# Performance work log

Hardware: AMD Instinct MI355X
Metric: run time of the kernel (lower is better)

## Reference

```python
import jax, jax.numpy as jnp
import numpy as np

N_NODES = 50000
N_EDGES = 800000
NFEAT, NHID, NCLASS = 512, 128, 40
BN_EPS = 1e-5


def setup_inputs() -> dict:
    key = jax.random.key(0)
    ks = jax.random.split(key, 12)
    x = jax.random.normal(ks[0], (N_NODES, NFEAT), dtype=jnp.float32)
    edge_index = jax.random.randint(ks[1], (2, N_EDGES), 0, N_NODES, dtype=jnp.int64)
    edge_weight = jax.random.uniform(ks[2], (N_EDGES,), dtype=jnp.float32)
    def glorot(k, fi, fo):
        lim = (6.0 / (fi + fo)) ** 0.5
        return jax.random.uniform(k, (fi, fo), minval=-lim, maxval=lim, dtype=jnp.float32)
    return {
        "x": x, "edge_index": edge_index, "edge_weight": edge_weight,
        "W1": glorot(ks[3], NFEAT, NHID), "b1": jnp.zeros((NHID,), jnp.float32),
        "W2": glorot(ks[4], NHID, NHID), "b2": jnp.zeros((NHID,), jnp.float32),
        "W3": glorot(ks[5], NHID, NHID), "b3": jnp.zeros((NHID,), jnp.float32),
        "g1": jnp.ones((NHID,), jnp.float32), "be1": jnp.zeros((NHID,), jnp.float32),
        "g2": jnp.ones((NHID,), jnp.float32), "be2": jnp.zeros((NHID,), jnp.float32),
        "g3": jnp.ones((NHID,), jnp.float32), "be3": jnp.zeros((NHID,), jnp.float32),
        "linW": glorot(ks[6], NHID, NCLASS), "linb": jnp.zeros((NCLASS,), jnp.float32),
    }


def _gcn_norm(edge_index, edge_weight, n):
    # PyG gcn_norm: add self-loops (weight 1), symmetric D^-1/2 (A+I) D^-1/2
    loop = jnp.arange(n, dtype=edge_index.dtype)
    row = jnp.concatenate([edge_index[0], loop])
    col = jnp.concatenate([edge_index[1], loop])
    ew = jnp.concatenate([edge_weight, jnp.ones((n,), edge_weight.dtype)])
    deg = jax.ops.segment_sum(ew, col, num_segments=n)
    dinv = jnp.where(deg > 0, jax.lax.rsqrt(jnp.maximum(deg, 1e-30)), 0.0)
    norm = dinv[row] * ew * dinv[col]
    return row, col, norm


def _conv(x, W, b, row, col, norm, n):
    h = x @ W                                   # [N, out]
    msg = h[row] * norm[:, None]                # gather + weight, [E+N, out]
    return jax.ops.segment_sum(msg, col, num_segments=n) + b


def _bn(x, g, b):
    # training-mode BatchNorm over node dim (biased variance)
    mu = jnp.mean(x, axis=0)
    var = jnp.mean((x - mu) ** 2, axis=0)
    return (x - mu) * jax.lax.rsqrt(var + BN_EPS) * g + b


def reference(x, edge_index, edge_weight, W1, b1, W2, b2, W3, b3,
              g1, be1, g2, be2, g3, be3, linW, linb):
    n = x.shape[0]
    row, col, norm = _gcn_norm(edge_index, edge_weight, n)
    x1 = _bn(jax.nn.relu(_conv(x, W1, b1, row, col, norm, n)), g1, be1)
    x2 = _bn(jax.nn.relu(_conv(x1, W2, b2, row, col, norm, n)), g2, be2)
    x3 = _bn(_conv(x2, W3, b3, row, col, norm, n), g3, be3)
    logits = x3 @ linW + linb
    return (logits, jax.nn.softmax(logits, axis=1), x3)
```

## Files before the change

kernel.cpp:

```cpp
#include <hip/hip_runtime.h>
#include <hip/hip_bf16.h>

#define N_NODES 50000
#define N_EDGES 800000
#define NFEAT 512
#define NHID 128
#define NCLASS 40
#define BN_EPS 1e-5f

typedef __attribute__((ext_vector_type(8))) short short8;
typedef __attribute__((ext_vector_type(4))) float f32x4;

__device__ __forceinline__ unsigned short f2b(float f) {
    unsigned int u = __float_as_uint(f);
    u += 0x7fff + ((u >> 16) & 1);
    return (unsigned short)(u >> 16);
}
__device__ __forceinline__ float blo(unsigned int v) {
    return __uint_as_float(v << 16);
}
__device__ __forceinline__ float bhi(unsigned int v) {
    return __uint_as_float(v & 0xffff0000u);
}

__global__ void k_detect(const unsigned int* __restrict__ words, int* __restrict__ flag) {
    __shared__ int s_any;
    if (threadIdx.x == 0) s_any = 0;
    __syncthreads();
    unsigned int v = words[2 * threadIdx.x + 1];
    if (v != 0) atomicAdd(&s_any, 1);
    __syncthreads();
    if (threadIdx.x == 0) *flag = (s_any == 0) ? 1 : 0;
}

__global__ void k_init_node(unsigned long long* __restrict__ degcnt) {
    int i = blockIdx.x * blockDim.x + threadIdx.x;
    if (i < N_NODES) degcnt[i] = 0ULL;
}

__global__ void k_convert_accum(const unsigned int* __restrict__ words,
                                const int* __restrict__ flag,
                                const float* __restrict__ ew,
                                int* __restrict__ row, int* __restrict__ col,
                                unsigned long long* __restrict__ degcnt,
                                int* __restrict__ slot) {
    int e = blockIdx.x * blockDim.x + threadIdx.x;
    if (e >= N_EDGES) return;
    int f = *flag;
    unsigned int r = f ? words[2 * (size_t)e] : words[e];
    unsigned int c = f ? words[2 * ((size_t)e + N_EDGES)] : words[e + N_EDGES];
    row[e] = (int)r;
    col[e] = (int)c;
    unsigned int q = __float2uint_rn(ew[e] * 8388608.0f);
    unsigned long long old = atomicAdd(&degcnt[c], (1ULL << 32) | (unsigned long long)q);
    slot[e] = (int)(old >> 32);
}

#define SCAN_BLOCKS ((N_NODES + 255) / 256)

__global__ __launch_bounds__(256) void k_dinv(const unsigned long long* __restrict__ degcnt,
                                              float* __restrict__ dinv,
                                              int* __restrict__ counts,
                                              int* __restrict__ bsum) {
    int i = blockIdx.x * 256 + threadIdx.x;
    int cnt = 0;
    if (i < N_NODES) {
        unsigned long long v = degcnt[i];
        float deg = 1.0f + (float)(unsigned int)(v & 0xffffffffULL) * (1.0f / 8388608.0f);
        dinv[i] = rsqrtf(deg);
        cnt = (int)(v >> 32);
        counts[i] = cnt;
    }
    __shared__ int sh[256];
    sh[threadIdx.x] = cnt;
    __syncthreads();
    for (int ofs = 128; ofs > 0; ofs >>= 1) {
        if (threadIdx.x < ofs) sh[threadIdx.x] += sh[threadIdx.x + ofs];
        __syncthreads();
    }
    if (threadIdx.x == 0) bsum[blockIdx.x] = sh[0];
}

__global__ __launch_bounds__(256) void k_scan2(const int* __restrict__ bsum,
                                               int* __restrict__ bpre,
                                               int* __restrict__ colptr) {
    int t = threadIdx.x;
    int v = (t < SCAN_BLOCKS) ? bsum[t] : 0;
    __shared__ int sh[256];
    sh[t] = v;
    __syncthreads();
    for (int ofs = 1; ofs < 256; ofs <<= 1) {
        int u = (t >= ofs) ? sh[t - ofs] : 0;
        __syncthreads();
        sh[t] += u;
        __syncthreads();
    }
    if (t < SCAN_BLOCKS) bpre[t] = sh[t] - v;
    if (t == SCAN_BLOCKS - 1) colptr[N_NODES] = sh[t];
}

__global__ __launch_bounds__(256) void k_scan3(const int* __restrict__ counts,
                                               const int* __restrict__ bpre,
                                               int* __restrict__ colptr) {
    int t = threadIdx.x;
    int i = blockIdx.x * 256 + t;
    int v = (i < N_NODES) ? counts[i] : 0;
    __shared__ int sh[256];
    sh[t] = v;
    __syncthreads();
    for (int ofs = 1; ofs < 256; ofs <<= 1) {
        int u = (t >= ofs) ? sh[t - ofs] : 0;
        __syncthreads();
        sh[t] += u;
        __syncthreads();
    }
    if (i < N_NODES) colptr[i] = bpre[blockIdx.x] + sh[t] - v;
}

__global__ void k_scatter(const int* __restrict__ row, const int* __restrict__ col,
                          const float* __restrict__ ew, const float* __restrict__ dinv,
                          const int* __restrict__ colptr, const int* __restrict__ slot,
                          int2* __restrict__ ern) {
    int e = blockIdx.x * blockDim.x + threadIdx.x;
    if (e < N_EDGES) {
        int c = col[e], r = row[e];
        int p = colptr[c] + slot[e];
        float nrm = dinv[r] * ew[e] * dinv[c];
        ern[p] = make_int2(r, __float_as_int(nrm));
    }
}

__global__ void k_prep_w(const float* __restrict__ W1, const float* __restrict__ W2,
                         const float* __restrict__ W3, unsigned short* __restrict__ W1t,
                         unsigned short* __restrict__ W2t, unsigned short* __restrict__ W3t) {
    int i = blockIdx.x * blockDim.x + threadIdx.x;
    if (i < 65536) {
        int k = i >> 7, n = i & 127;
        W1t[n * 512 + k] = f2b(W1[i]);
    } else if (i < 81920) {
        int j = i - 65536; int k = j >> 7, n = j & 127;
        W2t[n * 128 + k] = f2b(W2[j]);
    } else if (i < 98304) {
        int j = i - 81920; int k = j >> 7, n = j & 127;
        W3t[n * 128 + k] = f2b(W3[j]);
    }
}

template <int K, bool FUSE, bool ABF16>
__global__ __launch_bounds__(256) void k_gemm_bf16(
    const void* __restrict__ Av, const unsigned short* __restrict__ Wt,
    const float* __restrict__ scale, const float* __restrict__ shift,
    unsigned short* __restrict__ Out, int M) {
    __shared__ unsigned short As[128][40];
    __shared__ unsigned short Bs[128][40];
    __shared__ float s_sc[128], s_sh[128];
    int tid = threadIdx.x;
    int m0 = blockIdx.x * 128;
    if (FUSE) {
        if (tid < 128) { s_sc[tid] = scale[tid]; s_sh[tid] = shift[tid]; }
        __syncthreads();
    }
    int srow = tid >> 1;
    int skh = (tid & 1) << 4;
    int wave = tid >> 6, lane = tid & 63;
    int wm = (wave >> 1) * 64, wn = (wave & 1) * 64;
    int l15 = lane & 15, quad = lane >> 4;
    f32x4 acc[4][4] = {};
    bool arow_ok = (m0 + srow) < M;
    const float* arow_f = (const float*)Av + (size_t)(m0 + srow) * K + skh;
    const unsigned int* arow_b = (const unsigned int*)Av + (size_t)(m0 + srow) * (K / 2) + (skh >> 1);
    const unsigned short* wrow_p = Wt + (size_t)srow * K + skh;
    for (int kt = 0; kt < K; kt += 32) {
        unsigned int p[8];
        if (ABF16) {
            uint4 r0 = make_uint4(0, 0, 0, 0), r1 = make_uint4(0, 0, 0, 0);
            if (arow_ok) {
                r0 = *(const uint4*)(arow_b + (kt >> 1));
                r1 = *(const uint4*)(arow_b + (kt >> 1) + 4);
            }
            unsigned int raw[8] = {r0.x, r0.y, r0.z, r0.w, r1.x, r1.y, r1.z, r1.w};
#pragma unroll
            for (int q = 0; q < 8; q++) {
                if (FUSE) {
                    int ch = kt + skh + 2 * q;
                    float f0 = blo(raw[q]) * s_sc[ch] + s_sh[ch];
                    float f1 = bhi(raw[q]) * s_sc[ch + 1] + s_sh[ch + 1];
                    p[q] = (unsigned int)f2b(f0) | ((unsigned int)f2b(f1) << 16);
                } else {
                    p[q] = raw[q];
                }
            }
        } else {
            float v[16];
#pragma unroll
            for (int q = 0; q < 4; q++) {
                float4 t4 = make_float4(0.f, 0.f, 0.f, 0.f);
                if (arow_ok) t4 = *(const float4*)(arow_f + kt + q * 4);
                v[q * 4 + 0] = t4.x; v[q * 4 + 1] = t4.y;
                v[q * 4 + 2] = t4.z; v[q * 4 + 3] = t4.w;
            }
            if (FUSE) {
#pragma unroll
                for (int q = 0; q < 16; q++)
                    v[q] = v[q] * s_sc[kt + skh + q] + s_sh[kt + skh + q];
            }
#pragma unroll
            for (int q = 0; q < 8; q++)
                p[q] = (unsigned int)f2b(v[2 * q]) | ((unsigned int)f2b(v[2 * q + 1]) << 16);
        }
        uint4 w0 = make_uint4(p[0], p[1], p[2], p[3]);
        uint4 w1 = make_uint4(p[4], p[5], p[6], p[7]);
        uint4 b0 = *(const uint4*)(wrow_p + kt);
        uint4 b1 = *(const uint4*)(wrow_p + kt + 8);
        *(uint4*)&As[srow][skh] = w0;
        *(uint4*)&As[srow][skh + 8] = w1;
        *(uint4*)&Bs[srow][skh] = b0;
        *(uint4*)&Bs[srow][skh + 8] = b1;
        __syncthreads();
        short8 a[4], b[4];
#pragma unroll
        for (int i = 0; i < 4; i++) a[i] = *(const short8*)&As[wm + i * 16 + l15][quad * 8];
#pragma unroll
        for (int j = 0; j < 4; j++) b[j] = *(const short8*)&Bs[wn + j * 16 + l15][quad * 8];
#pragma unroll
        for (int i = 0; i < 4; i++)
#pragma unroll
            for (int j = 0; j < 4; j++)
                acc[i][j] = __builtin_amdgcn_mfma_f32_16x16x32_bf16(a[i], b[j], acc[i][j], 0, 0, 0);
        __syncthreads();
    }
#pragma unroll
    for (int i = 0; i < 4; i++) {
        int mb = m0 + wm + i * 16 + quad * 4;
#pragma unroll
        for (int r = 0; r < 4; r++) {
            int m = mb + r;
            if (m < M) {
#pragma unroll
                for (int j = 0; j < 4; j++)
                    Out[(size_t)m * 128 + wn + j * 16 + l15] = f2b(acc[i][j][r]);
            }
        }
    }
}

__global__ __launch_bounds__(256) void k_aggregate(
    const unsigned int* __restrict__ hb, const int* __restrict__ colptr,
    const int2* __restrict__ ern, const float* __restrict__ dinv,
    const float* __restrict__ bias, unsigned int* __restrict__ out, int relu) {
    int node = (blockIdx.x * blockDim.x + threadIdx.x) >> 6;
    int lane = threadIdx.x & 63;
    if (node >= N_NODES) return;
    float di = dinv[node];
    float selfw = di * di;
    unsigned int sv = hb[(size_t)node * 64 + lane];
    float a0 = selfw * blo(sv);
    float a1 = selfw * bhi(sv);
    float c0 = 0.f, c1 = 0.f;
    int e = colptr[node], end = colptr[node + 1];
    for (; e + 8 <= end; e += 8) {
        int2 rw[8];
#pragma unroll
        for (int q = 0; q < 8; q++) rw[q] = ern[e + q];
        unsigned int v[8];
#pragma unroll
        for (int q = 0; q < 8; q++) v[q] = hb[(size_t)rw[q].x * 64 + lane];
#pragma unroll
        for (int q = 0; q < 8; q++) {
            float w = __int_as_float(rw[q].y);
            if (q & 1) { c0 += w * blo(v[q]); c1 += w * bhi(v[q]); }
            else       { a0 += w * blo(v[q]); a1 += w * bhi(v[q]); }
        }
    }
    for (; e < end; e++) {
        int2 rw = ern[e];
        float w = __int_as_float(rw.y);
        unsigned int v = hb[(size_t)rw.x * 64 + lane];
        a0 += w * blo(v);
        a1 += w * bhi(v);
    }
    a0 += c0; a1 += c1;
    float2 bv = *(const float2*)&bias[2 * lane];
    a0 += bv.x;
    a1 += bv.y;
    if (relu) { a0 = fmaxf(a0, 0.f); a1 = fmaxf(a1, 0.f); }
    out[(size_t)node * 64 + lane] = (unsigned int)f2b(a0) | ((unsigned int)f2b(a1) << 16);
}

#define BN_BLOCKS ((N_NODES + 255) / 256)

__global__ __launch_bounds__(256) void k_bnstats(const unsigned int* __restrict__ x,
                                                 float* __restrict__ psum,
                                                 float* __restrict__ psumsq) {
    int u = threadIdx.x & 63;
    int strip = threadIdx.x >> 6;
    int r0 = blockIdx.x * 256;
    int rend = min(r0 + 256, N_NODES);
    float sl = 0.f, s2l = 0.f, sh_ = 0.f, s2h = 0.f;
    for (int r = r0 + strip; r < rend; r += 4) {
        unsigned int v = x[(size_t)r * 64 + u];
        float a = blo(v), b = bhi(v);
        sl += a; s2l += a * a;
        sh_ += b; s2h += b * b;
    }
    __shared__ float buf[4][64][4];
    buf[strip][u][0] = sl; buf[strip][u][1] = s2l;
    buf[strip][u][2] = sh_; buf[strip][u][3] = s2h;
    __syncthreads();
    if (strip == 0) {
#pragma unroll
        for (int s = 1; s < 4; s++) {
            sl += buf[s][u][0]; s2l += buf[s][u][1];
            sh_ += buf[s][u][2]; s2h += buf[s][u][3];
        }
        psum[blockIdx.x * 128 + 2 * u] = sl;
        psum[blockIdx.x * 128 + 2 * u + 1] = sh_;
        psumsq[blockIdx.x * 128 + 2 * u] = s2l;
        psumsq[blockIdx.x * 128 + 2 * u + 1] = s2h;
    }
}

__global__ void k_bnfinal(const float* __restrict__ psum, const float* __restrict__ psumsq,
                          const float* __restrict__ g, const float* __restrict__ be,
                          float* __restrict__ scale, float* __restrict__ shift) {
    int c = threadIdx.x;
    if (c < 128) {
        float s = 0.f, s2 = 0.f;
        for (int b = 0; b < BN_BLOCKS; b++) {
            s += psum[b * 128 + c];
            s2 += psumsq[b * 128 + c];
        }
        const float invn = 1.0f / (float)N_NODES;
        float mu = s * invn;
        float var = s2 * invn - mu * mu;
        float iv = rsqrtf(var + BN_EPS);
        float sc = g[c] * iv;
        scale[c] = sc;
        shift[c] = be[c] - mu * sc;
    }
}

__global__ __launch_bounds__(256) void k_logits(const unsigned int* __restrict__ abuf,
                                                const float* __restrict__ scale,
                                                const float* __restrict__ shift,
                                                const float* __restrict__ linW,
                                                const float* __restrict__ linb,
                                                float* __restrict__ logits,
                                                float* __restrict__ probs,
                                                float* __restrict__ x3out) {
    __shared__ float Xs[64][130];
    __shared__ float Ws[128 * 40];
    __shared__ float s_sc[128], s_sh[128];
    int tid = threadIdx.x;
    int m0 = blockIdx.x * 64;
    if (tid < 128) { s_sc[tid] = scale[tid]; s_sh[tid] = shift[tid]; }
    for (int q = tid; q < 1280; q += 256)
        *(float4*)&Ws[q * 4] = *(const float4*)&linW[q * 4];
    __syncthreads();
    for (int q = tid; q < 4096; q += 256) {
        int r = q >> 6, u = q & 63;
        int m = m0 + r;
        float f0 = 0.f, f1 = 0.f;
        if (m < N_NODES) {
            unsigned int v = abuf[(size_t)m * 64 + u];
            f0 = blo(v) * s_sc[2 * u] + s_sh[2 * u];
            f1 = bhi(v) * s_sc[2 * u + 1] + s_sh[2 * u + 1];
            *(float2*)&x3out[(size_t)m * 128 + 2 * u] = make_float2(f0, f1);
        }
        *(float2*)&Xs[r][2 * u] = make_float2(f0, f1);
    }
    __syncthreads();
    int r = tid >> 2;
    int cg = tid & 3;
    int cbase = cg * 10;
    float acc[10] = {};
    for (int k = 0; k < 128; k++) {
        float a = Xs[r][k];
#pragma unroll
        for (int j = 0; j < 10; j++) acc[j] += a * Ws[k * 40 + cbase + j];
    }
#pragma unroll
    for (int j = 0; j < 10; j++) acc[j] += linb[cbase + j];
    float m = acc[0];
#pragma unroll
    for (int j = 1; j < 10; j++) m = fmaxf(m, acc[j]);
    m = fmaxf(m, __shfl_xor(m, 1));
    m = fmaxf(m, __shfl_xor(m, 2));
    float ex[10];
    float s = 0.f;
#pragma unroll
    for (int j = 0; j < 10; j++) { ex[j] = expf(acc[j] - m); s += ex[j]; }
    s += __shfl_xor(s, 1);
    s += __shfl_xor(s, 2);
    float inv = 1.0f / s;
    int mrow = m0 + r;
    if (mrow < N_NODES) {
#pragma unroll
        for (int j = 0; j < 10; j++) {
            logits[(size_t)mrow * 40 + cbase + j] = acc[j];
            probs[(size_t)mrow * 40 + cbase + j] = ex[j] * inv;
        }
    }
}

extern "C" void kernel_launch(void* const* d_in, const int* in_sizes, int n_in,
                              void* d_out, int out_size, void* d_ws, size_t ws_size,
                              hipStream_t stream) {
    const float* x = (const float*)d_in[0];
    const unsigned int* eidx = (const unsigned int*)d_in[1];
    const float* ew = (const float*)d_in[2];
    const float* W1 = (const float*)d_in[3];
    const float* b1 = (const float*)d_in[4];
    const float* W2 = (const float*)d_in[5];
    const float* b2 = (const float*)d_in[6];
    const float* W3 = (const float*)d_in[7];
    const float* b3 = (const float*)d_in[8];
    const float* g1 = (const float*)d_in[9];
    const float* be1 = (const float*)d_in[10];
    const float* g2 = (const float*)d_in[11];
    const float* be2 = (const float*)d_in[12];
    const float* g3 = (const float*)d_in[13];
    const float* be3 = (const float*)d_in[14];
    const float* linW = (const float*)d_in[15];
    const float* linb = (const float*)d_in[16];

    float* out = (float*)d_out;
    float* logits = out;
    float* probs = out + (size_t)N_NODES * NCLASS;
    float* x3out = out + 2 * (size_t)N_NODES * NCLASS;

    char* ws = (char*)d_ws;
    size_t off = 0;
    auto take = [&](size_t bytes) -> char* {
        char* p = ws + off;
        off += (bytes + 255) & ~(size_t)255;
        return p;
    };
    int* row32 = (int*)take((size_t)N_EDGES * 4);
    int* col32 = (int*)take((size_t)N_EDGES * 4);
    int* slot = (int*)take((size_t)N_EDGES * 4);
    int* colptr = (int*)take((size_t)(N_NODES + 1) * 4);
    int* counts = (int*)take((size_t)N_NODES * 4);
    unsigned long long* degcnt = (unsigned long long*)take((size_t)N_NODES * 8);
    int2* ern = (int2*)take((size_t)N_EDGES * 8);
    float* dinv = (float*)take((size_t)N_NODES * 4);
    unsigned short* hbuf = (unsigned short*)take((size_t)N_NODES * NHID * 2);
    unsigned short* abuf = (unsigned short*)take((size_t)N_NODES * NHID * 2);
    unsigned short* W1t = (unsigned short*)take((size_t)512 * 128 * 2);
    unsigned short* W2t = (unsigned short*)take((size_t)128 * 128 * 2);
    unsigned short* W3t = (unsigned short*)take((size_t)128 * 128 * 2);
    float* psum = (float*)take((size_t)BN_BLOCKS * 128 * 4);
    float* psumsq = (float*)take((size_t)BN_BLOCKS * 128 * 4);
    float* scale = (float*)take(128 * 4);
    float* shift = (float*)take(128 * 4);
    int* bsum = (int*)take((size_t)SCAN_BLOCKS * 4);
    int* bpre = (int*)take((size_t)SCAN_BLOCKS * 4);
    int* flag = (int*)take(4);
    (void)ws_size; (void)n_in; (void)in_sizes; (void)out_size;

    const int TPB = 256;
    int grid_e = (N_EDGES + TPB - 1) / TPB;
    int grid_gemm = (N_NODES + 127) / 128;
    int grid_agg = (N_NODES * 64 + TPB - 1) / TPB;
    int grid_head = (N_NODES + 63) / 64;

    k_detect<<<1, 256, 0, stream>>>(eidx, flag);
    k_init_node<<<SCAN_BLOCKS, TPB, 0, stream>>>(degcnt);
    k_convert_accum<<<grid_e, TPB, 0, stream>>>(eidx, flag, ew, row32, col32, degcnt, slot);
    k_dinv<<<SCAN_BLOCKS, TPB, 0, stream>>>(degcnt, dinv, counts, bsum);
    k_scan2<<<1, TPB, 0, stream>>>(bsum, bpre, colptr);
    k_scan3<<<SCAN_BLOCKS, TPB, 0, stream>>>(counts, bpre, colptr);
    k_scatter<<<grid_e, TPB, 0, stream>>>(row32, col32, ew, dinv, colptr, slot, ern);
    k_prep_w<<<(98304 + TPB - 1) / TPB, TPB, 0, stream>>>(W1, W2, W3, W1t, W2t, W3t);

    k_gemm_bf16<NFEAT, false, false><<<grid_gemm, TPB, 0, stream>>>(x, W1t, nullptr, nullptr, hbuf, N_NODES);
    k_aggregate<<<grid_agg, TPB, 0, stream>>>((const unsigned int*)hbuf, colptr, ern, dinv, b1, (unsigned int*)abuf, 1);
    k_bnstats<<<BN_BLOCKS, TPB, 0, stream>>>((const unsigned int*)abuf, psum, psumsq);
    k_bnfinal<<<1, 128, 0, stream>>>(psum, psumsq, g1, be1, scale, shift);

    k_gemm_bf16<NHID, true, true><<<grid_gemm, TPB, 0, stream>>>(abuf, W2t, scale, shift, hbuf, N_NODES);
    k_aggregate<<<grid_agg, TPB, 0, stream>>>((const unsigned int*)hbuf, colptr, ern, dinv, b2, (unsigned int*)abuf, 1);
    k_bnstats<<<BN_BLOCKS, TPB, 0, stream>>>((const unsigned int*)abuf, psum, psumsq);
    k_bnfinal<<<1, 128, 0, stream>>>(psum, psumsq, g2, be2, scale, shift);

    k_gemm_bf16<NHID, true, true><<<grid_gemm, TPB, 0, stream>>>(abuf, W3t, scale, shift, hbuf, N_NODES);
    k_aggregate<<<grid_agg, TPB, 0, stream>>>((const unsigned int*)hbuf, colptr, ern, dinv, b3, (unsigned int*)abuf, 0);
    k_bnstats<<<BN_BLOCKS, TPB, 0, stream>>>((const unsigned int*)abuf, psum, psumsq);
    k_bnfinal<<<1, 128, 0, stream>>>(psum, psumsq, g3, be3, scale, shift);

    k_logits<<<grid_head, TPB, 0, stream>>>((const unsigned int*)abuf, scale, shift, linW, linb, logits, probs, x3out);
}
```

Before: 526.0 us.

## Fuse GEMM1 with edge conversion, atomic BN stats, fold BN finalize into consumers

Merges the first-layer GEMM and the edge-index conversion/degree accumulation into one launch with block-range dispatch, so the independent graph-preprocessing work can overlap the dense GEMM. The separate detect kernel is folded into each edge block, which repeats the format probe per block. BN statistics now go through float atomics into a single 128-wide sum buffer zeroed by the aggregate kernel, and the per-channel scale/shift finalize is recomputed inside the next GEMM and the logits kernel. This removes the bnfinal launches and partial-sum buffers, at the cost of atomic contention and order-dependent float summation.

Result: faster. 494.6 us (-6.0%).

```diff
diff --git a/kernel.cpp b/kernel.cpp
--- a/kernel.cpp
+++ b/kernel.cpp
@@ -11,6 +11,11 @@
 typedef __attribute__((ext_vector_type(8))) short short8;
 typedef __attribute__((ext_vector_type(4))) float f32x4;
 
+#define GEMM1_BLOCKS ((N_NODES + 127) / 128)
+#define EDGE_BLOCKS ((N_EDGES + 255) / 256)
+#define SCAN_BLOCKS ((N_NODES + 255) / 256)
+#define BN_BLOCKS ((N_NODES + 255) / 256)
+
 __device__ __forceinline__ unsigned short f2b(float f) {
     unsigned int u = __float_as_uint(f);
     u += 0x7fff + ((u >> 16) & 1);
@@ -23,111 +28,9 @@
     return __uint_as_float(v & 0xffff0000u);
 }
 
-__global__ void k_detect(const unsigned int* __restrict__ words, int* __restrict__ flag) {
-    __shared__ int s_any;
-    if (threadIdx.x == 0) s_any = 0;
-    __syncthreads();
-    unsigned int v = words[2 * threadIdx.x + 1];
-    if (v != 0) atomicAdd(&s_any, 1);
-    __syncthreads();
-    if (threadIdx.x == 0) *flag = (s_any == 0) ? 1 : 0;
-}
-
 __global__ void k_init_node(unsigned long long* __restrict__ degcnt) {
     int i = blockIdx.x * blockDim.x + threadIdx.x;
     if (i < N_NODES) degcnt[i] = 0ULL;
-}
-
-__global__ void k_convert_accum(const unsigned int* __restrict__ words,
-                                const int* __restrict__ flag,
-                                const float* __restrict__ ew,
-                                int* __restrict__ row, int* __restrict__ col,
-                                unsigned long long* __restrict__ degcnt,
-                                int* __restrict__ slot) {
-    int e = blockIdx.x * blockDim.x + threadIdx.x;
-    if (e >= N_EDGES) return;
-    int f = *flag;
-    unsigned int r = f ? words[2 * (size_t)e] : words[e];
-    unsigned int c = f ? words[2 * ((size_t)e + N_EDGES)] : words[e + N_EDGES];
-    row[e] = (int)r;
-    col[e] = (int)c;
-    unsigned int q = __float2uint_rn(ew[e] * 8388608.0f);
-    unsigned long long old = atomicAdd(&degcnt[c], (1ULL << 32) | (unsigned long long)q);
-    slot[e] = (int)(old >> 32);
-}
-
-#define SCAN_BLOCKS ((N_NODES + 255) / 256)
-
-__global__ __launch_bounds__(256) void k_dinv(const unsigned long long* __restrict__ degcnt,
-                                              float* __restrict__ dinv,
-                                              int* __restrict__ counts,
-                                              int* __restrict__ bsum) {
-    int i = blockIdx.x * 256 + threadIdx.x;
-    int cnt = 0;
-    if (i < N_NODES) {
-        unsigned long long v = degcnt[i];
-        float deg = 1.0f + (float)(unsigned int)(v & 0xffffffffULL) * (1.0f / 8388608.0f);
-        dinv[i] = rsqrtf(deg);
-        cnt = (int)(v >> 32);
-        counts[i] = cnt;
-    }
-    __shared__ int sh[256];
-    sh[threadIdx.x] = cnt;
-    __syncthreads();
-    for (int ofs = 128; ofs > 0; ofs >>= 1) {
-        if (threadIdx.x < ofs) sh[threadIdx.x] += sh[threadIdx.x + ofs];
-        __syncthreads();
-    }
-    if (threadIdx.x == 0) bsum[blockIdx.x] = sh[0];
-}
-
-__global__ __launch_bounds__(256) void k_scan2(const int* __restrict__ bsum,
-                                               int* __restrict__ bpre,
-                                               int* __restrict__ colptr) {
-    int t = threadIdx.x;
-    int v = (t < SCAN_BLOCKS) ? bsum[t] : 0;
-    __shared__ int sh[256];
-    sh[t] = v;
-    __syncthreads();
-    for (int ofs = 1; ofs < 256; ofs <<= 1) {
-        int u = (t >= ofs) ? sh[t - ofs] : 0;
-        __syncthreads();
-        sh[t] += u;
-        __syncthreads();
-    }
-    if (t < SCAN_BLOCKS) bpre[t] = sh[t] - v;
-    if (t == SCAN_BLOCKS - 1) colptr[N_NODES] = sh[t];
-}
-
-__global__ __launch_bounds__(256) void k_scan3(const int* __restrict__ counts,
-                                               const int* __restrict__ bpre,
-                                               int* __restrict__ colptr) {
-    int t = threadIdx.x;
-    int i = blockIdx.x * 256 + t;
-    int v = (i < N_NODES) ? counts[i] : 0;
-    __shared__ int sh[256];
-    sh[t] = v;
-    __syncthreads();
-    for (int ofs = 1; ofs < 256; ofs <<= 1) {
-        int u = (t >= ofs) ? sh[t - ofs] : 0;
-        __syncthreads();
-        sh[t] += u;
-        __syncthreads();
-    }
-    if (i < N_NODES) colptr[i] = bpre[blockIdx.x] + sh[t] - v;
-}
-
-__global__ void k_scatter(const int* __restrict__ row, const int* __restrict__ col,
-                          const float* __restrict__ ew, const float* __restrict__ dinv,
-                          const int* __restrict__ colptr, const int* __restrict__ slot,
-                          int2* __restrict__ ern) {
-    int e = blockIdx.x * blockDim.x + threadIdx.x;
-    if (e < N_EDGES) {
-        int c = col[e], r = row[e];
-        int p = colptr[c] + slot[e];
-        float nrm = dinv[r] * ew[e] * dinv[c];
-        ern[p] = make_int2(r, __float_as_int(nrm));
-    }
 }
 
 __global__ void k_prep_w(const float* __restrict__ W1, const float* __restrict__ W2,
@@ -146,108 +49,175 @@
     }
 }
 
-template <int K, bool FUSE, bool ABF16>
-__global__ __launch_bounds__(256) void k_gemm_bf16(
-    const void* __restrict__ Av, const unsigned short* __restrict__ Wt,
-    const float* __restrict__ scale, const float* __restrict__ shift,
-    unsigned short* __restrict__ Out, int M) {
+__global__ __launch_bounds__(256) void k_fat(
+    const float* __restrict__ x, const unsigned short* __restrict__ W1t,
+    unsigned short* __restrict__ hbuf,
+    const unsigned int* __restrict__ words, const float* __restrict__ ew,
+    int* __restrict__ row, int* __restrict__ col,
+    unsigned long long* __restrict__ degcnt, int* __restrict__ slot) {
     __shared__ unsigned short As[128][40];
     __shared__ unsigned short Bs[128][40];
-    __shared__ float s_sc[128], s_sh[128];
+    __shared__ int s_any;
     int tid = threadIdx.x;
-    int m0 = blockIdx.x * 128;
-    if (FUSE) {
-        if (tid < 128) { s_sc[tid] = scale[tid]; s_sh[tid] = shift[tid]; }
-        __syncthreads();
-    }
-    int srow = tid >> 1;
-    int skh = (tid & 1) << 4;
-    int wave = tid >> 6, lane = tid & 63;
-    int wm = (wave >> 1) * 64, wn = (wave & 1) * 64;
-    int l15 = lane & 15, quad = lane >> 4;
-    f32x4 acc[4][4] = {};
-    bool arow_ok = (m0 + srow) < M;
-    const float* arow_f = (const float*)Av + (size_t)(m0 + srow) * K + skh;
-    const unsigned int* arow_b = (const unsigned int*)Av + (size_t)(m0 + srow) * (K / 2) + (skh >> 1);
-    const unsigned short* wrow_p = Wt + (size_t)srow * K + skh;
-    for (int kt = 0; kt < K; kt += 32) {
-        unsigned int p[8];
-        if (ABF16) {
-            uint4 r0 = make_uint4(0, 0, 0, 0), r1 = make_uint4(0, 0, 0, 0);
-            if (arow_ok) {
-                r0 = *(const uint4*)(arow_b + (kt >> 1));
-                r1 = *(const uint4*)(arow_b + (kt >> 1) + 4);
-            }
-            unsigned int raw[8] = {r0.x, r0.y, r0.z, r0.w, r1.x, r1.y, r1.z, r1.w};
-#pragma unroll
-            for (int q = 0; q < 8; q++) {
-                if (FUSE) {
-                    int ch = kt + skh + 2 * q;
-                    float f0 = blo(raw[q]) * s_sc[ch] + s_sh[ch];
-                    float f1 = bhi(raw[q]) * s_sc[ch + 1] + s_sh[ch + 1];
-                    p[q] = (unsigned int)f2b(f0) | ((unsigned int)f2b(f1) << 16);
-                } else {
-                    p[q] = raw[q];
-                }
-            }
-        } else {
+    if (blockIdx.x < GEMM1_BLOCKS) {
+        int m0 = blockIdx.x * 128;
+        int srow = tid >> 1;
+        int skh = (tid & 1) << 4;
+        int wave = tid >> 6, lane = tid & 63;
+        int wm = (wave >> 1) * 64, wn = (wave & 1) * 64;
+        int l15 = lane & 15, quad = lane >> 4;
+        f32x4 acc[4][4] = {};
+        bool arow_ok = (m0 + srow) < N_NODES;
+        const float* arow_p = x + (size_t)(m0 + srow) * 512 + skh;
+        const unsigned short* wrow_p = W1t + (size_t)srow * 512 + skh;
+        for (int kt = 0; kt < 512; kt += 32) {
             float v[16];
 #pragma unroll
             for (int q = 0; q < 4; q++) {
                 float4 t4 = make_float4(0.f, 0.f, 0.f, 0.f);
-                if (arow_ok) t4 = *(const float4*)(arow_f + kt + q * 4);
+                if (arow_ok) t4 = *(const float4*)(arow_p + kt + q * 4);
                 v[q * 4 + 0] = t4.x; v[q * 4 + 1] = t4.y;
                 v[q * 4 + 2] = t4.z; v[q * 4 + 3] = t4.w;
             }
-            if (FUSE) {
-#pragma unroll
-                for (int q = 0; q < 16; q++)
-                    v[q] = v[q] * s_sc[kt + skh + q] + s_sh[kt + skh + q];
-            }
+            unsigned int p[8];
 #pragma unroll
             for (int q = 0; q < 8; q++)
                 p[q] = (unsigned int)f2b(v[2 * q]) | ((unsigned int)f2b(v[2 * q + 1]) << 16);
-        }
-        uint4 w0 = make_uint4(p[0], p[1], p[2], p[3]);
-        uint4 w1 = make_uint4(p[4], p[5], p[6], p[7]);
-        uint4 b0 = *(const uint4*)(wrow_p + kt);
-        uint4 b1 = *(const uint4*)(wrow_p + kt + 8);
-        *(uint4*)&As[srow][skh] = w0;
-        *(uint4*)&As[srow][skh + 8] = w1;
-        *(uint4*)&Bs[srow][skh] = b0;
-        *(uint4*)&Bs[srow][skh + 8] = b1;
-        __syncthreads();
-        short8 a[4], b[4];
-#pragma unroll
-        for (int i = 0; i < 4; i++) a[i] = *(const short8*)&As[wm + i * 16 + l15][quad * 8];
-#pragma unroll
-        for (int j = 0; j < 4; j++) b[j] = *(const short8*)&Bs[wn + j * 16 + l15][quad * 8];
-#pragma unroll
-        for (int i = 0; i < 4; i++)
-#pragma unroll
-            for (int j = 0; j < 4; j++)
-                acc[i][j] = __builtin_amdgcn_mfma_f32_16x16x32_bf16(a[i], b[j], acc[i][j], 0, 0, 0);
-        __syncthreads();
-    }
-#pragma unroll
-    for (int i = 0; i < 4; i++) {
-        int mb = m0 + wm + i * 16 + quad * 4;
-#pragma unroll
-        for (int r = 0; r < 4; r++) {
-            int m = mb + r;
-            if (m < M) {
+            uint4 w0 = make_uint4(p[0], p[1], p[2], p[3]);
+            uint4 w1 = make_uint4(p[4], p[5], p[6], p[7]);
+            uint4 b0 = *(const uint4*)(wrow_p + kt);
+            uint4 b1 = *(const uint4*)(wrow_p + kt + 8);
+            *(uint4*)&As[srow][skh] = w0;
+            *(uint4*)&As[srow][skh + 8] = w1;
+            *(uint4*)&Bs[srow][skh] = b0;
+            *(uint4*)&Bs[srow][skh + 8] = b1;
+            __syncthreads();
+            short8 a[4], b[4];
+#pragma unroll
+            for (int i = 0; i < 4; i++) a[i] = *(const short8*)&As[wm + i * 16 + l15][quad * 8];
+#pragma unroll
+            for (int j = 0; j < 4; j++) b[j] = *(const short8*)&Bs[wn + j * 16 + l15][quad * 8];
+#pragma unroll
+            for (int i = 0; i < 4; i++)
 #pragma unroll
                 for (int j = 0; j < 4; j++)
-                    Out[(size_t)m * 128 + wn + j * 16 + l15] = f2b(acc[i][j][r]);
+                    acc[i][j] = __builtin_amdgcn_mfma_f32_16x16x32_bf16(a[i], b[j], acc[i][j], 0, 0, 0);
+            __syncthreads();
+        }
+#pragma unroll
+        for (int i = 0; i < 4; i++) {
+            int mb = m0 + wm + i * 16 + quad * 4;
+#pragma unroll
+            for (int r = 0; r < 4; r++) {
+                int m = mb + r;
+                if (m < N_NODES) {
+#pragma unroll
+                    for (int j = 0; j < 4; j++)
+                        hbuf[(size_t)m * 128 + wn + j * 16 + l15] = f2b(acc[i][j][r]);
+                }
             }
         }
+    } else {
+        if (tid == 0) s_any = 0;
+        __syncthreads();
+        unsigned int probe = words[2 * tid + 1];
+        if (probe != 0) atomicAdd(&s_any, 1);
+        __syncthreads();
+        int f = (s_any == 0) ? 1 : 0;
+        int e = (blockIdx.x - GEMM1_BLOCKS) * 256 + tid;
+        if (e < N_EDGES) {
+            unsigned int r = f ? words[2 * (size_t)e] : words[e];
+            unsigned int c = f ? words[2 * ((size_t)e + N_EDGES)] : words[e + N_EDGES];
+            row[e] = (int)r;
+            col[e] = (int)c;
+            unsigned int q = __float2uint_rn(ew[e] * 8388608.0f);
+            unsigned long long old = atomicAdd(&degcnt[c], (1ULL << 32) | (unsigned long long)q);
+            slot[e] = (int)(old >> 32);
+        }
+    }
+}
+
+__global__ __launch_bounds__(256) void k_dinv(const unsigned long long* __restrict__ degcnt,
+                                              float* __restrict__ dinv,
+                                              int* __restrict__ counts,
+                                              int* __restrict__ bsum) {
+    int i = blockIdx.x * 256 + threadIdx.x;
+    int cnt = 0;
+    if (i < N_NODES) {
+        unsigned long long v = degcnt[i];
+        float deg = 1.0f + (float)(unsigned int)(v & 0xffffffffULL) * (1.0f / 8388608.0f);
+        dinv[i] = rsqrtf(deg);
+        cnt = (int)(v >> 32);
+        counts[i] = cnt;
+    }
+    __shared__ int sh[256];
+    sh[threadIdx.x] = cnt;
+    __syncthreads();
+    for (int ofs = 128; ofs > 0; ofs >>= 1) {
+        if (threadIdx.x < ofs) sh[threadIdx.x] += sh[threadIdx.x + ofs];
+        __syncthreads();
+    }
+    if (threadIdx.x == 0) bsum[blockIdx.x] = sh[0];
+}
+
+__global__ __launch_bounds__(256) void k_scan2(const int* __restrict__ bsum,
+                                               int* __restrict__ bpre,
+                                               int* __restrict__ colptr) {
+    int t = threadIdx.x;
+    int v = (t < SCAN_BLOCKS) ? bsum[t] : 0;
+    __shared__ int sh[256];
+    sh[t] = v;
+    __syncthreads();
+    for (int ofs = 1; ofs < 256; ofs <<= 1) {
+        int u = (t >= ofs) ? sh[t - ofs] : 0;
+        __syncthreads();
+        sh[t] += u;
+        __syncthreads();
+    }
+    if (t < SCAN_BLOCKS) bpre[t] = sh[t] - v;
+    if (t == SCAN_BLOCKS - 1) colptr[N_NODES] = sh[t];
+}
+
+__global__ __launch_bounds__(256) void k_scan3(const int* __restrict__ counts,
+                                               const int* __restrict__ bpre,
+                                               int* __restrict__ colptr) {
+    int t = threadIdx.x;
+    int i = blockIdx.x * 256 + t;
+    int v = (i < N_NODES) ? counts[i] : 0;
+    __shared__ int sh[256];
+    sh[t] = v;
+    __syncthreads();
+    for (int ofs = 1; ofs < 256; ofs <<= 1) {
+        int u = (t >= ofs) ? sh[t - ofs] : 0;
+        __syncthreads();
+        sh[t] += u;
+        __syncthreads();
+    }
+    if (i < N_NODES) colptr[i] = bpre[blockIdx.x] + sh[t] - v;
+}
+
+__global__ void k_scatter(const int* __restrict__ row, const int* __restrict__ col,
+                          const float* __restrict__ ew, const float* __restrict__ dinv,
+                          const int* __restrict__ colptr, const int* __restrict__ slot,
+                          int2* __restrict__ ern) {
+    int e = blockIdx.x * blockDim.x + threadIdx.x;
+    if (e < N_EDGES) {
+        int c = col[e], r = row[e];
+        int p = colptr[c] + slot[e];
+        float nrm = dinv[r] * ew[e] * dinv[c];
+        ern[p] = make_int2(r, __float_as_int(nrm));
     }
 }
 
 __global__ __launch_bounds__(256) void k_aggregate(
     const unsigned int* __restrict__ hb, const int* __restrict__ colptr,
     const int2* __restrict__ ern, const float* __restrict__ dinv,
-    const float* __restrict__ bias, unsigned int* __restrict__ out, int relu) {
+    const float* __restrict__ bias, unsigned int* __restrict__ out, int relu,
+    float* __restrict__ sums, float* __restrict__ sumsq) {
+    if (blockIdx.x == 0) {
+        if (threadIdx.x < 128) sums[threadIdx.x] = 0.f;
+        else sumsq[threadIdx.x - 128] = 0.f;
+    }
     int node = (blockIdx.x * blockDim.x + threadIdx.x) >> 6;
     int lane = threadIdx.x & 63;
     if (node >= N_NODES) return;
@@ -287,11 +257,9 @@
     out[(size_t)node * 64 + lane] = (unsigned int)f2b(a0) | ((unsigned int)f2b(a1) << 16);
 }
 
-#define BN_BLOCKS ((N_NODES + 255) / 256)
-
 __global__ __launch_bounds__(256) void k_bnstats(const unsigned int* __restrict__ x,
-                                                 float* __restrict__ psum,
-                                                 float* __restrict__ psumsq) {
+                                                 float* __restrict__ sums,
+                                                 float* __restrict__ sumsq) {
     int u = threadIdx.x & 63;
     int strip = threadIdx.x >> 6;
     int r0 = blockIdx.x * 256;
@@ -313,36 +281,98 @@
             sl += buf[s][u][0]; s2l += buf[s][u][1];
             sh_ += buf[s][u][2]; s2h += buf[s][u][3];
         }
-        psum[blockIdx.x * 128 + 2 * u] = sl;
-        psum[blockIdx.x * 128 + 2 * u + 1] = sh_;
-        psumsq[blockIdx.x * 128 + 2 * u] = s2l;
-        psumsq[blockIdx.x * 128 + 2 * u + 1] = s2h;
-    }
-}
-
-__global__ void k_bnfinal(const float* __restrict__ psum, const float* __restrict__ psumsq,
-                          const float* __restrict__ g, const float* __restrict__ be,
-                          float* __restrict__ scale, float* __restrict__ shift) {
-    int c = threadIdx.x;
-    if (c < 128) {
-        float s = 0.f, s2 = 0.f;
-        for (int b = 0; b < BN_BLOCKS; b++) {
-            s += psum[b * 128 + c];
-            s2 += psumsq[b * 128 + c];
-        }
+        atomicAdd(&sums[2 * u], sl);
+        atomicAdd(&sums[2 * u + 1], sh_);
+        atomicAdd(&sumsq[2 * u], s2l);
+        atomicAdd(&sumsq[2 * u + 1], s2h);
+    }
+}
+
+__global__ __launch_bounds__(256) void k_gemm_h(
+    const unsigned int* __restrict__ Ab, const unsigned short* __restrict__ Wt,
+    const float* __restrict__ sums, const float* __restrict__ sumsq,
+    const float* __restrict__ g, const float* __restrict__ be,
+    unsigned short* __restrict__ Out) {
+    __shared__ unsigned short As[128][40];
+    __shared__ unsigned short Bs[128][40];
+    __shared__ float s_sc[128], s_sh[128];
+    int tid = threadIdx.x;
+    int m0 = blockIdx.x * 128;
+    if (tid < 128) {
         const float invn = 1.0f / (float)N_NODES;
-        float mu = s * invn;
-        float var = s2 * invn - mu * mu;
+        float mu = sums[tid] * invn;
+        float var = sumsq[tid] * invn - mu * mu;
         float iv = rsqrtf(var + BN_EPS);
-        float sc = g[c] * iv;
-        scale[c] = sc;
-        shift[c] = be[c] - mu * sc;
+        float sc = g[tid] * iv;
+        s_sc[tid] = sc;
+        s_sh[tid] = be[tid] - mu * sc;
+    }
+    __syncthreads();
+    int srow = tid >> 1;
+    int skh = (tid & 1) << 4;
+    int wave = tid >> 6, lane = tid & 63;
+    int wm = (wave >> 1) * 64, wn = (wave & 1) * 64;
+    int l15 = lane & 15, quad = lane >> 4;
+    f32x4 acc[4][4] = {};
+    bool arow_ok = (m0 + srow) < N_NODES;
+    const unsigned int* arow_b = Ab + (size_t)(m0 + srow) * 64 + (skh >> 1);
+    const unsigned short* wrow_p = Wt + (size_t)srow * 128 + skh;
+    for (int kt = 0; kt < 128; kt += 32) {
+        uint4 r0 = make_uint4(0, 0, 0, 0), r1 = make_uint4(0, 0, 0, 0);
+        if (arow_ok) {
+            r0 = *(const uint4*)(arow_b + (kt >> 1));
+            r1 = *(const uint4*)(arow_b + (kt >> 1) + 4);
+        }
+        unsigned int raw[8] = {r0.x, r0.y, r0.z, r0.w, r1.x, r1.y, r1.z, r1.w};
+        unsigned int p[8];
+#pragma unroll
+        for (int q = 0; q < 8; q++) {
+            int ch = kt + skh + 2 * q;
+            float f0 = blo(raw[q]) * s_sc[ch] + s_sh[ch];
+            float f1 = bhi(raw[q]) * s_sc[ch + 1] + s_sh[ch + 1];
+            p[q] = (unsigned int)f2b(f0) | ((unsigned int)f2b(f1) << 16);
+        }
+        uint4 w0 = make_uint4(p[0], p[1], p[2], p[3]);
+        uint4 w1 = make_uint4(p[4], p[5], p[6], p[7]);
+        uint4 b0 = *(const uint4*)(wrow_p + kt);
+        uint4 b1 = *(const uint4*)(wrow_p + kt + 8);
+        *(uint4*)&As[srow][skh] = w0;
+        *(uint4*)&As[srow][skh + 8] = w1;
+        *(uint4*)&Bs[srow][skh] = b0;
+        *(uint4*)&Bs[srow][skh + 8] = b1;
+        __syncthreads();
+        short8 a[4], b[4];
+#pragma unroll
+        for (int i = 0; i < 4; i++) a[i] = *(const short8*)&As[wm + i * 16 + l15][quad * 8];
+#pragma unroll
+        for (int j = 0; j < 4; j++) b[j] = *(const short8*)&Bs[wn + j * 16 + l15][quad * 8];
+#pragma unroll
+        for (int i = 0; i < 4; i++)
+#pragma unroll
+            for (int j = 0; j < 4; j++)
+                acc[i][j] = __builtin_amdgcn_mfma_f32_16x16x32_bf16(a[i], b[j], acc[i][j], 0, 0, 0);
+        __syncthreads();
+    }
+#pragma unroll
+    for (int i = 0; i < 4; i++) {
+        int mb = m0 + wm + i * 16 + quad * 4;
+#pragma unroll
+        for (int r = 0; r < 4; r++) {
+            int m = mb + r;
+            if (m < N_NODES) {
+#pragma unroll
+                for (int j = 0; j < 4; j++)
+                    Out[(size_t)m * 128 + wn + j * 16 + l15] = f2b(acc[i][j][r]);
+            }
+        }
     }
 }
 
 __global__ __launch_bounds__(256) void k_logits(const unsigned int* __restrict__ abuf,
-                                                const float* __restrict__ scale,
-                                                const float* __restrict__ shift,
+                                                const float* __restrict__ sums,
+                                                const float* __restrict__ sumsq,
+                                                const float* __restrict__ g,
+                                                const float* __restrict__ be,
                                                 const float* __restrict__ linW,
                                                 const float* __restrict__ linb,
                                                 float* __restrict__ logits,
@@ -353,7 +383,15 @@
     __shared__ float s_sc[128], s_sh[128];
     int tid = threadIdx.x;
     int m0 = blockIdx.x * 64;
-    if (tid < 128) { s_sc[tid] = scale[tid]; s_sh[tid] = shift[tid]; }
+    if (tid < 128) {
+        const float invn = 1.0f / (float)N_NODES;
+        float mu = sums[tid] * invn;
+        float var = sumsq[tid] * invn - mu * mu;
+        float iv = rsqrtf(var + BN_EPS);
+        float sc = g[tid] * iv;
+        s_sc[tid] = sc;
+        s_sh[tid] = be[tid] - mu * sc;
+    }
     for (int q = tid; q < 1280; q += 256)
         *(float4*)&Ws[q * 4] = *(const float4*)&linW[q * 4];
     __syncthreads();
@@ -449,44 +487,37 @@
     unsigned short* W1t = (unsigned short*)take((size_t)512 * 128 * 2);
     unsigned short* W2t = (unsigned short*)take((size_t)128 * 128 * 2);
     unsigned short* W3t = (unsigned short*)take((size_t)128 * 128 * 2);
-    float* psum = (float*)take((size_t)BN_BLOCKS * 128 * 4);
-    float* psumsq = (float*)take((size_t)BN_BLOCKS * 128 * 4);
-    float* scale = (float*)take(128 * 4);
-    float* shift = (float*)take(128 * 4);
+    float* sums = (float*)take(128 * 4);
+    float* sumsq = (float*)take(128 * 4);
     int* bsum = (int*)take((size_t)SCAN_BLOCKS * 4);
     int* bpre = (int*)take((size_t)SCAN_BLOCKS * 4);
-    int* flag = (int*)take(4);
     (void)ws_size; (void)n_in; (void)in_sizes; (void)out_size;
 
     const int TPB = 256;
-    int grid_e = (N_EDGES + TPB - 1) / TPB;
-    int grid_gemm = (N_NODES + 127) / 128;
+    int grid_e = EDGE_BLOCKS;
+    int grid_gemm = GEMM1_BLOCKS;
     int grid_agg = (N_NODES * 64 + TPB - 1) / TPB;
     int grid_head = (N_NODES + 63) / 64;
 
-    k_detect<<<1, 256, 0, stream>>>(eidx, flag);
     k_init_node<<<SCAN_BLOCKS, TPB, 0, stream>>>(degcnt);
-    k_convert_accum<<<grid_e, TPB, 0, stream>>>(eidx, flag, ew, row32, col32, degcnt, slot);
+    k_prep_w<<<(98304 + TPB - 1) / TPB, TPB, 0, stream>>>(W1, W2, W3, W1t, W2t, W3t);
+    k_fat<<<GEMM1_BLOCKS + EDGE_BLOCKS, TPB, 0, stream>>>(
+        x, W1t, hbuf, eidx, ew, row32, col32, degcnt, slot);
     k_dinv<<<SCAN_BLOCKS, TPB, 0, stream>>>(degcnt, dinv, counts, bsum);
     k_scan2<<<1, TPB, 0, stream>>>(bsum, bpre, colptr);
     k_scan3<<<SCAN_BLOCKS, TPB, 0, stream>>>(counts, bpre, colptr);
     k_scatter<<<grid_e, TPB, 0, stream>>>(row32, col32, ew, dinv, colptr, slot, ern);
-    k_prep_w<<<(98304 + TPB - 1) / TPB, TPB, 0, stream>>>(W1, W2, W3, W1t, W2t, W3t);
-
-    k_gemm_bf16<NFEAT, false, false><<<grid_gemm, TPB, 0, stream>>>(x, W1t, nullptr, nullptr, hbuf, N_NODES);
-    k_aggregate<<<grid_agg, TPB, 0, stream>>>((const unsigned int*)hbuf, colptr, ern, dinv, b1, (unsigned int*)abuf, 1);
-    k_bnstats<<<BN_BLOCKS, TPB, 0, stream>>>((const unsigned int*)abuf, psum, psumsq);
-    k_bnfinal<<<1, 128, 0, stream>>>(psum, psumsq, g1, be1, scale, shift);
-
-    k_gemm_bf16<NHID, true, true><<<grid_gemm, TPB, 0, stream>>>(abuf, W2t, scale, shift, hbuf, N_NODES);
-    k_aggregate<<<grid_agg, TPB, 0, stream>>>((const unsigned int*)hbuf, colptr, ern, dinv, b2, (unsigned int*)abuf, 1);
-    k_bnstats<<<BN_BLOCKS, TPB, 0, stream>>>((const unsigned int*)abuf, psum, psumsq);
-    k_bnfinal<<<1, 128, 0, stream>>>(psum, psumsq, g2, be2, scale, shift);
-
-    k_gemm_bf16<NHID, true, true><<<grid_gemm, TPB, 0, stream>>>(abuf, W3t, scale, shift, hbuf, N_NODES);
-    k_aggregate<<<grid_agg, TPB, 0, stream>>>((const unsigned int*)hbuf, colptr, ern, dinv, b3, (unsigned int*)abuf, 0);
-    k_bnstats<<<BN_BLOCKS, TPB, 0, stream>>>((const unsigned int*)abuf, psum, psumsq);
-    k_bnfinal<<<1, 128, 0, stream>>>(psum, psumsq, g3, be3, scale, shift);
-
-    k_logits<<<grid_head, TPB, 0, stream>>>((const unsigned int*)abuf, scale, shift, linW, linb, logits, probs, x3out);
-}
+
+    k_aggregate<<<grid_agg, TPB, 0, stream>>>((const unsigned int*)hbuf, colptr, ern, dinv, b1, (unsigned int*)abuf, 1, sums, sumsq);
+    k_bnstats<<<BN_BLOCKS, TPB, 0, stream>>>((const unsigned int*)abuf, sums, sumsq);
+
+    k_gemm_h<<<grid_gemm, TPB, 0, stream>>>((const unsigned int*)abuf, W2t, sums, sumsq, g1, be1, hbuf);
+    k_aggregate<<<grid_agg, TPB, 0, stream>>>((const unsigned int*)hbuf, colptr, ern, dinv, b2, (unsigned int*)abuf, 1, sums, sumsq);
+    k_bnstats<<<BN_BLOCKS, TPB, 0, stream>>>((const unsigned int*)abuf, sums, sumsq);
+
+    k_gemm_h<<<grid_gemm, TPB, 0, stream>>>((const unsigned int*)abuf, W3t, sums, sumsq, g2, be2, hbuf);
+    k_aggregate<<<grid_agg, TPB, 0, stream>>>((const unsigned int*)hbuf, colptr, ern, dinv, b3, (unsigned int*)abuf, 0, sums, sumsq);
+    k_bnstats<<<BN_BLOCKS, TPB, 0, stream>>>((const unsigned int*)abuf, sums, sumsq);
+
+    k_logits<<<grid_head, TPB, 0, stream>>>((const unsigned int*)abuf, sums, sumsq, g3, be3, linW, linb, logits, probs, x3out);
+}
```
